# Performance work log

Hardware: AMD Instinct MI355X
Metric: run time of the kernel (lower is better)

Reference implementation:

```python
import jax, jax.numpy as jnp
import numpy as np

MAXDISP = 192
DOWNSAMPLE = 4
NUM_GROUPS = 40
D = MAXDISP // DOWNSAMPLE  # 48 disparity bins


def setup_inputs() -> dict:
    key = jax.random.key(0)
    k1, k2, k3, k4 = jax.random.split(key, 4)
    return {
        "ref_gwc": jax.random.normal(k1, (1, 320, 128, 240), jnp.float32),
        "tgt_gwc": jax.random.normal(k2, (1, 320, 128, 240), jnp.float32),
        "ref_concat": jax.random.normal(k3, (1, 12, 128, 240), jnp.float32),
        "tgt_concat": jax.random.normal(k4, (1, 12, 128, 240), jnp.float32),
    }


def _shift_right(x, d):
    # target feature shifted right by disparity d, zero-filled on the left
    if d == 0:
        return x
    W = x.shape[-1]
    return jnp.pad(x[..., : W - d], ((0, 0), (0, 0), (0, 0), (d, 0)))


def reference(ref_gwc, tgt_gwc, ref_concat, tgt_concat):
    B, C, H, W = ref_gwc.shape
    cpg = C // NUM_GROUPS  # channels per group
    w = jnp.arange(W)

    # Groupwise-correlation volume [B, G, D, H, W].
    # Shifted tgt is zero for w < d, so product is zero there (matches torch zeros init).
    gwc = jnp.stack(
        [
            (ref_gwc * _shift_right(tgt_gwc, d))
            .reshape(B, NUM_GROUPS, cpg, H, W)
            .mean(axis=2)
            for d in range(D)
        ],
        axis=2,
    )

    # Concat volume [B, 2*Cc, D, H, W]; ref half must also be zero for w < d.
    cat_slices = []
    for d in range(D):
        mask = (w >= d).astype(ref_concat.dtype)  # [W]
        cat_slices.append(
            jnp.concatenate([ref_concat * mask, _shift_right(tgt_concat, d)], axis=1)
        )
    concat_vol = jnp.stack(cat_slices, axis=2)

    return jnp.concatenate([gwc, concat_vol], axis=1)  # [B, G+2*Cc, D, H, W]
```

## Files before the change

kernel.cpp:

```cpp
#include <hip/hip_runtime.h>

constexpr int W   = 240;
constexpr int H   = 128;
constexpr int D   = 48;
constexpr int G   = 40;
constexpr int CPG = 8;
constexpr int CC  = 12;
constexpr int HW  = H * W;
constexpr int PAD = 48;
constexpr int TROW = PAD + W;

constexpr int NGWC = G * H;
constexpr int NCAT = 2 * CC * H;
constexpr int NGRID = NGWC + NCAT;

__device__ __forceinline__ void nt_store4(float* p, float4 v) {
  __builtin_nontemporal_store(v.x, p + 0);
  __builtin_nontemporal_store(v.y, p + 1);
  __builtin_nontemporal_store(v.z, p + 2);
  __builtin_nontemporal_store(v.w, p + 3);
}

__global__ __launch_bounds__(256) void fused_kernel(const float* __restrict__ ref,
                                                    const float* __restrict__ tgt,
                                                    const float* __restrict__ refc,
                                                    const float* __restrict__ tgtc,
                                                    float* __restrict__ out) {
  __shared__ float sref[CPG][W];
  __shared__ float stgt[CPG][TROW];

  const int bid = blockIdx.x;
  const int grp = bid >> 3;
  const int rr  = bid & 7;
  const int tid = threadIdx.x;

  const int lane = tid & 63;
  const int dq   = tid >> 6;
  const int w4   = lane;
  const int d0   = dq * 12;

  if (rr < 5) {
    const int aid = grp * 5 + rr;
    const int g   = aid >> 7;
    const int h   = aid & (H - 1);

    for (int p = tid; p < CPG * (PAD / 4); p += 256) {
      int c = p / (PAD / 4);
      int i = p - c * (PAD / 4);
      *(float4*)&stgt[c][i * 4] = make_float4(0.f, 0.f, 0.f, 0.f);
    }
    const size_t rowbase = (size_t)(g * CPG) * HW + (size_t)h * W;
    for (int q = tid; q < CPG * (W / 4); q += 256) {
      int c  = q / (W / 4);
      int x4 = q - c * (W / 4);
      float4 rv = *(const float4*)&ref[rowbase + (size_t)c * HW + x4 * 4];
      float4 tv = *(const float4*)&tgt[rowbase + (size_t)c * HW + x4 * 4];
      *(float4*)&sref[c][x4 * 4]       = rv;
      *(float4*)&stgt[c][PAD + x4 * 4] = tv;
    }
    __syncthreads();
    if (w4 >= W / 4) return;

    float4 acc[12];
#pragma unroll
    for (int j = 0; j < 12; ++j) acc[j] = make_float4(0.f, 0.f, 0.f, 0.f);

    const int base = 4 * w4 - d0 - 12;
#pragma unroll
    for (int c = 0; c < CPG; ++c) {
      float4 r = *(const float4*)&sref[c][4 * w4];
      const float4* tp = (const float4*)&stgt[c][PAD + base];
      float tt[16];
      *(float4*)&tt[0]  = tp[0];
      *(float4*)&tt[4]  = tp[1];
      *(float4*)&tt[8]  = tp[2];
      *(float4*)&tt[12] = tp[3];
#pragma unroll
      for (int j = 0; j < 12; ++j) {
        acc[j].x += r.x * tt[12 - j];
        acc[j].y += r.y * tt[13 - j];
        acc[j].z += r.z * tt[14 - j];
        acc[j].w += r.w * tt[15 - j];
      }
    }

    float* op = out + ((size_t)(g * D + d0) * H + h) * W + 4 * w4;
#pragma unroll
    for (int j = 0; j < 12; ++j) {
      nt_store4(op, make_float4(acc[j].x * 0.125f, acc[j].y * 0.125f,
                                acc[j].z * 0.125f, acc[j].w * 0.125f));
      op += HW;
    }
  } else {
    const int cid = grp * 3 + (rr - 5);
    const int c2  = cid >> 7;
    const int h   = cid & (H - 1);
    float* srow = &stgt[0][0];

    if (tid < PAD / 4)
      *(float4*)&srow[tid * 4] = make_float4(0.f, 0.f, 0.f, 0.f);
    const bool is_ref = (c2 < CC);
    const float* src = is_ref ? (refc + (size_t)c2 * HW + (size_t)h * W)
                              : (tgtc + (size_t)(c2 - CC) * HW + (size_t)h * W);
    if (tid < W / 4)
      *(float4*)&srow[PAD + tid * 4] = *(const float4*)&src[tid * 4];
    __syncthreads();
    if (w4 >= W / 4) return;

    float* op = out + ((size_t)((G + c2) * D + d0) * H + h) * W + 4 * w4;
    if (is_ref) {
      const float4 rv = *(const float4*)&srow[PAD + 4 * w4];
      const int w0 = 4 * w4;
#pragma unroll
      for (int j = 0; j < 12; ++j) {
        const int d = d0 + j;
        float4 v;
        v.x = (w0 + 0 >= d) ? rv.x : 0.f;
        v.y = (w0 + 1 >= d) ? rv.y : 0.f;
        v.z = (w0 + 2 >= d) ? rv.z : 0.f;
        v.w = (w0 + 3 >= d) ? rv.w : 0.f;
        nt_store4(op, v);
        op += HW;
      }
    } else {
      const int base = 4 * w4 - d0 - 12;
      const float4* tp = (const float4*)&srow[PAD + base];
      float tt[16];
      *(float4*)&tt[0]  = tp[0];
      *(float4*)&tt[4]  = tp[1];
      *(float4*)&tt[8]  = tp[2];
      *(float4*)&tt[12] = tp[3];
#pragma unroll
      for (int j = 0; j < 12; ++j) {
        nt_store4(op, make_float4(tt[12 - j], tt[13 - j], tt[14 - j], tt[15 - j]));
        op += HW;
      }
    }
  }
}

extern "C" void kernel_launch(void* const* d_in, const int* in_sizes, int n_in,
                              void* d_out, int out_size, void* d_ws, size_t ws_size,
                              hipStream_t stream) {
  const float* ref_gwc    = (const float*)d_in[0];
  const float* tgt_gwc    = (const float*)d_in[1];
  const float* ref_concat = (const float*)d_in[2];
  const float* tgt_concat = (const float*)d_in[3];
  float* out = (float*)d_out;

  fused_kernel<<<NGRID, 256, 0, stream>>>(ref_gwc, tgt_gwc, ref_concat,
                                          tgt_concat, out);
}
```

Baseline: 85.81 us.

## Process 8 rows per block with double-buffered register prefetch of next row

Each block now handles 8 consecutive H rows instead of one, cutting the grid from 8192 to 1024 blocks. The next row's inputs are prefetched into registers while the current row is computed and stored, then written into a second shared-memory buffer, so loads overlap compute and stores. This saves per-block launch and setup cost. The trade-offs are fewer blocks in flight (parallelism to hide store latency), doubled shared memory, and a barrier per row.

```diff
diff --git a/kernel.cpp b/kernel.cpp
--- a/kernel.cpp
+++ b/kernel.cpp
@@ -10,8 +10,10 @@
 constexpr int PAD = 48;
 constexpr int TROW = PAD + W;
 
-constexpr int NGWC = G * H;
-constexpr int NCAT = 2 * CC * H;
+constexpr int HC   = 8;
+constexpr int NHC  = H / HC;
+constexpr int NGWC = G * NHC;
+constexpr int NCAT = 2 * CC * NHC;
 constexpr int NGRID = NGWC + NCAT;
 
 __device__ __forceinline__ void nt_store4(float* p, float4 v) {
@@ -26,8 +28,8 @@
                                                     const float* __restrict__ refc,
                                                     const float* __restrict__ tgtc,
                                                     float* __restrict__ out) {
-  __shared__ float sref[CPG][W];
-  __shared__ float stgt[CPG][TROW];
+  __shared__ float sref[2][CPG][W];
+  __shared__ float stgt[2][CPG][TROW];
 
   const int bid = blockIdx.x;
   const int grp = bid >> 3;
@@ -41,100 +43,161 @@
 
   if (rr < 5) {
     const int aid = grp * 5 + rr;
-    const int g   = aid >> 7;
-    const int h   = aid & (H - 1);
-
-    for (int p = tid; p < CPG * (PAD / 4); p += 256) {
-      int c = p / (PAD / 4);
-      int i = p - c * (PAD / 4);
-      *(float4*)&stgt[c][i * 4] = make_float4(0.f, 0.f, 0.f, 0.f);
-    }
-    const size_t rowbase = (size_t)(g * CPG) * HW + (size_t)h * W;
-    for (int q = tid; q < CPG * (W / 4); q += 256) {
-      int c  = q / (W / 4);
-      int x4 = q - c * (W / 4);
-      float4 rv = *(const float4*)&ref[rowbase + (size_t)c * HW + x4 * 4];
-      float4 tv = *(const float4*)&tgt[rowbase + (size_t)c * HW + x4 * 4];
-      *(float4*)&sref[c][x4 * 4]       = rv;
-      *(float4*)&stgt[c][PAD + x4 * 4] = tv;
+    const int g   = aid >> 4;
+    const int h0  = (aid & 15) * HC;
+
+    for (int p = tid; p < 2 * CPG * (PAD / 4); p += 256) {
+      int b = p / (CPG * (PAD / 4));
+      int r = p - b * (CPG * (PAD / 4));
+      int c = r / (PAD / 4);
+      int i = r - c * (PAD / 4);
+      *(float4*)&stgt[b][c][i * 4] = make_float4(0.f, 0.f, 0.f, 0.f);
+    }
+
+    const int  q0c = tid / (W / 4), q0x = tid - q0c * (W / 4);
+    const int  q1  = tid + 256;
+    const bool q1v = q1 < CPG * (W / 4);
+    const int  q1c = q1 / (W / 4), q1x = q1 - q1c * (W / 4);
+
+    const size_t gbase = (size_t)(g * CPG) * HW;
+    const size_t a0 = gbase + (size_t)q0c * HW + q0x * 4;
+    const size_t a1 = gbase + (size_t)q1c * HW + q1x * 4;
+
+    {
+      const size_t hoff = (size_t)h0 * W;
+      float4 rv0 = *(const float4*)&ref[a0 + hoff];
+      float4 tv0 = *(const float4*)&tgt[a0 + hoff];
+      *(float4*)&sref[0][q0c][q0x * 4]       = rv0;
+      *(float4*)&stgt[0][q0c][PAD + q0x * 4] = tv0;
+      if (q1v) {
+        float4 rv1 = *(const float4*)&ref[a1 + hoff];
+        float4 tv1 = *(const float4*)&tgt[a1 + hoff];
+        *(float4*)&sref[0][q1c][q1x * 4]       = rv1;
+        *(float4*)&stgt[0][q1c][PAD + q1x * 4] = tv1;
+      }
     }
     __syncthreads();
-    if (w4 >= W / 4) return;
-
-    float4 acc[12];
-#pragma unroll
-    for (int j = 0; j < 12; ++j) acc[j] = make_float4(0.f, 0.f, 0.f, 0.f);
-
-    const int base = 4 * w4 - d0 - 12;
-#pragma unroll
-    for (int c = 0; c < CPG; ++c) {
-      float4 r = *(const float4*)&sref[c][4 * w4];
-      const float4* tp = (const float4*)&stgt[c][PAD + base];
-      float tt[16];
-      *(float4*)&tt[0]  = tp[0];
-      *(float4*)&tt[4]  = tp[1];
-      *(float4*)&tt[8]  = tp[2];
-      *(float4*)&tt[12] = tp[3];
-#pragma unroll
-      for (int j = 0; j < 12; ++j) {
-        acc[j].x += r.x * tt[12 - j];
-        acc[j].y += r.y * tt[13 - j];
-        acc[j].z += r.z * tt[14 - j];
-        acc[j].w += r.w * tt[15 - j];
-      }
-    }
-
-    float* op = out + ((size_t)(g * D + d0) * H + h) * W + 4 * w4;
-#pragma unroll
-    for (int j = 0; j < 12; ++j) {
-      nt_store4(op, make_float4(acc[j].x * 0.125f, acc[j].y * 0.125f,
-                                acc[j].z * 0.125f, acc[j].w * 0.125f));
-      op += HW;
+
+    for (int hh = 0; hh < HC; ++hh) {
+      const int  b  = hh & 1;
+      const bool pf = (hh + 1 < HC);
+      float4 rv0, tv0, rv1, tv1;
+      if (pf) {
+        const size_t hoff = (size_t)(h0 + hh + 1) * W;
+        rv0 = *(const float4*)&ref[a0 + hoff];
+        tv0 = *(const float4*)&tgt[a0 + hoff];
+        if (q1v) {
+          rv1 = *(const float4*)&ref[a1 + hoff];
+          tv1 = *(const float4*)&tgt[a1 + hoff];
+        }
+      }
+
+      if (w4 < W / 4) {
+        float4 acc[12];
+#pragma unroll
+        for (int j = 0; j < 12; ++j) acc[j] = make_float4(0.f, 0.f, 0.f, 0.f);
+
+        const int base = 4 * w4 - d0 - 12;
+#pragma unroll
+        for (int c = 0; c < CPG; ++c) {
+          float4 r = *(const float4*)&sref[b][c][4 * w4];
+          const float4* tp = (const float4*)&stgt[b][c][PAD + base];
+          float tt[16];
+          *(float4*)&tt[0]  = tp[0];
+          *(float4*)&tt[4]  = tp[1];
+          *(float4*)&tt[8]  = tp[2];
+          *(float4*)&tt[12] = tp[3];
+#pragma unroll
+          for (int j = 0; j < 12; ++j) {
+            acc[j].x += r.x * tt[12 - j];
+            acc[j].y += r.y * tt[13 - j];
+            acc[j].z += r.z * tt[14 - j];
+            acc[j].w += r.w * tt[15 - j];
+          }
+        }
+
+        float* op = out + ((size_t)(g * D + d0) * H + (h0 + hh)) * W + 4 * w4;
+#pragma unroll
+        for (int j = 0; j < 12; ++j) {
+          nt_store4(op, make_float4(acc[j].x * 0.125f, acc[j].y * 0.125f,
+                                    acc[j].z * 0.125f, acc[j].w * 0.125f));
+          op += HW;
+        }
+      }
+
+      if (pf) {
+        *(float4*)&sref[b ^ 1][q0c][q0x * 4]       = rv0;
+        *(float4*)&stgt[b ^ 1][q0c][PAD + q0x * 4] = tv0;
+        if (q1v) {
+          *(float4*)&sref[b ^ 1][q1c][q1x * 4]       = rv1;
+          *(float4*)&stgt[b ^ 1][q1c][PAD + q1x * 4] = tv1;
+        }
+      }
+      __syncthreads();
     }
   } else {
     const int cid = grp * 3 + (rr - 5);
-    const int c2  = cid >> 7;
-    const int h   = cid & (H - 1);
-    float* srow = &stgt[0][0];
-
-    if (tid < PAD / 4)
-      *(float4*)&srow[tid * 4] = make_float4(0.f, 0.f, 0.f, 0.f);
+    const int c2  = cid >> 4;
+    const int h0  = (cid & 15) * HC;
     const bool is_ref = (c2 < CC);
-    const float* src = is_ref ? (refc + (size_t)c2 * HW + (size_t)h * W)
-                              : (tgtc + (size_t)(c2 - CC) * HW + (size_t)h * W);
+    const float* src = is_ref ? (refc + (size_t)c2 * HW)
+                              : (tgtc + (size_t)(c2 - CC) * HW);
+
+    if (tid < 2 * (PAD / 4)) {
+      int b = tid / (PAD / 4);
+      int i = tid - b * (PAD / 4);
+      *(float4*)&stgt[b][0][i * 4] = make_float4(0.f, 0.f, 0.f, 0.f);
+    }
     if (tid < W / 4)
-      *(float4*)&srow[PAD + tid * 4] = *(const float4*)&src[tid * 4];
+      *(float4*)&stgt[0][0][PAD + tid * 4] =
+          *(const float4*)&src[(size_t)h0 * W + tid * 4];
     __syncthreads();
-    if (w4 >= W / 4) return;
-
-    float* op = out + ((size_t)((G + c2) * D + d0) * H + h) * W + 4 * w4;
-    if (is_ref) {
-      const float4 rv = *(const float4*)&srow[PAD + 4 * w4];
-      const int w0 = 4 * w4;
-#pragma unroll
-      for (int j = 0; j < 12; ++j) {
-        const int d = d0 + j;
-        float4 v;
-        v.x = (w0 + 0 >= d) ? rv.x : 0.f;
-        v.y = (w0 + 1 >= d) ? rv.y : 0.f;
-        v.z = (w0 + 2 >= d) ? rv.z : 0.f;
-        v.w = (w0 + 3 >= d) ? rv.w : 0.f;
-        nt_store4(op, v);
-        op += HW;
-      }
-    } else {
-      const int base = 4 * w4 - d0 - 12;
-      const float4* tp = (const float4*)&srow[PAD + base];
-      float tt[16];
-      *(float4*)&tt[0]  = tp[0];
-      *(float4*)&tt[4]  = tp[1];
-      *(float4*)&tt[8]  = tp[2];
-      *(float4*)&tt[12] = tp[3];
-#pragma unroll
-      for (int j = 0; j < 12; ++j) {
-        nt_store4(op, make_float4(tt[12 - j], tt[13 - j], tt[14 - j], tt[15 - j]));
-        op += HW;
-      }
+
+    for (int hh = 0; hh < HC; ++hh) {
+      const int  b  = hh & 1;
+      const bool pf = (hh + 1 < HC);
+      float4 nv;
+      if (pf && tid < W / 4)
+        nv = *(const float4*)&src[(size_t)(h0 + hh + 1) * W + tid * 4];
+
+      if (w4 < W / 4) {
+        const float* srow = &stgt[b][0][0];
+        float* op =
+            out + ((size_t)((G + c2) * D + d0) * H + (h0 + hh)) * W + 4 * w4;
+        if (is_ref) {
+          const float4 rv = *(const float4*)&srow[PAD + 4 * w4];
+          const int w0 = 4 * w4;
+#pragma unroll
+          for (int j = 0; j < 12; ++j) {
+            const int d = d0 + j;
+            float4 v;
+            v.x = (w0 + 0 >= d) ? rv.x : 0.f;
+            v.y = (w0 + 1 >= d) ? rv.y : 0.f;
+            v.z = (w0 + 2 >= d) ? rv.z : 0.f;
+            v.w = (w0 + 3 >= d) ? rv.w : 0.f;
+            nt_store4(op, v);
+            op += HW;
+          }
+        } else {
+          const int base = 4 * w4 - d0 - 12;
+          const float4* tp = (const float4*)&srow[PAD + base];
+          float tt[16];
+          *(float4*)&tt[0]  = tp[0];
+          *(float4*)&tt[4]  = tp[1];
+          *(float4*)&tt[8]  = tp[2];
+          *(float4*)&tt[12] = tp[3];
+#pragma unroll
+          for (int j = 0; j < 12; ++j) {
+            nt_store4(op,
+                      make_float4(tt[12 - j], tt[13 - j], tt[14 - j], tt[15 - j]));
+            op += HW;
+          }
+        }
+      }
+
+      if (pf && tid < W / 4)
+        *(float4*)&stgt[b ^ 1][0][PAD + tid * 4] = nv;
+      __syncthreads();
     }
   }
 }
```

Measured after the change: 90.34 us. 5.3% more time.
